# Optimization experiments

Measured on AMD Instinct MI355X. Metric: run time of the kernel, lower is better.

Reference implementation:

```python
import jax, jax.numpy as jnp
import numpy as np

B, T, D, H = 4, 2048, 1024, 16
DH = D // H  # 64
EPS = 1e-5


def _layernorm(x, g, b):
    mu = jnp.mean(x, axis=-1, keepdims=True)
    var = jnp.var(x, axis=-1, keepdims=True)
    return (x - mu) * jax.lax.rsqrt(var + EPS) * g + b


def setup_inputs() -> dict:
    key = jax.random.key(0)
    ks = jax.random.split(key, 12)
    s = 0.02
    x = jax.random.normal(ks[0], (B, T, D), dtype=jnp.float32)
    # causal mask (the repo registers tril as the eos_mask buffer)
    eos_mask = jnp.broadcast_to(jnp.tril(jnp.ones((T, T), dtype=jnp.int32)), (B, T, T))
    Wq = jax.random.normal(ks[1], (H, D, DH), dtype=jnp.float32) * s
    Wk = jax.random.normal(ks[2], (H, D, DH), dtype=jnp.float32) * s
    Wv = jax.random.normal(ks[3], (H, D, DH), dtype=jnp.float32) * s
    Wp = jax.random.normal(ks[4], (D, D), dtype=jnp.float32) * s
    bp = jnp.zeros((D,), dtype=jnp.float32)
    W1 = jax.random.normal(ks[5], (D, 4 * D), dtype=jnp.float32) * s
    b1 = jnp.zeros((4 * D,), dtype=jnp.float32)
    W2 = jax.random.normal(ks[6], (4 * D, D), dtype=jnp.float32) * s
    b2 = jnp.zeros((D,), dtype=jnp.float32)
    g1 = jnp.ones((D,), dtype=jnp.float32)
    beta1 = jnp.zeros((D,), dtype=jnp.float32)
    g2 = jnp.ones((D,), dtype=jnp.float32)
    beta2 = jnp.zeros((D,), dtype=jnp.float32)
    return dict(x=x, eos_mask=eos_mask, Wq=Wq, Wk=Wk, Wv=Wv, Wp=Wp, bp=bp,
                W1=W1, b1=b1, W2=W2, b2=b2, g1=g1, beta1=beta1, g2=g2, beta2=beta2)


def reference(x, eos_mask, Wq, Wk, Wv, Wp, bp, W1, b1, W2, b2, g1, beta1, g2, beta2):
    # x: [B,T,D]; eos_mask: [B,T,T]
    x1 = _layernorm(x, g1, beta1)
    q = jnp.einsum('btd,hdk->bhtk', x1, Wq)
    k = jnp.einsum('btd,hdk->bhtk', x1, Wk)
    v = jnp.einsum('btd,hdk->bhtk', x1, Wv)
    # NOTE: original scales by 1/sqrt(C) where C = d_model (not d_head)
    scores = jnp.einsum('bhtk,bhsk->bhts', q, k) / np.sqrt(x.shape[-1]).astype(np.float32)
    scores = jnp.where(eos_mask[:, None, :, :] == 0, jnp.float32(-jnp.inf), scores)
    wei = jax.nn.softmax(scores, axis=-1)
    attn = jnp.einsum('bhts,bhsk->bhtk', wei, v)          # [B,H,T,DH]
    attn = attn.transpose(0, 2, 1, 3).reshape(x.shape)    # concat heads -> [B,T,D]
    attn = attn @ Wp + bp
    x2 = x1 + attn
    x3 = _layernorm(x2, g2, beta2)
    mlp = jax.nn.relu(x3 @ W1 + b1) @ W2 + b2
    out = x3 + mlp
    return out
```

## Files before the change

kernel.cpp:

```cpp
#include <hip/hip_runtime.h>


#define B_ 4
#define T_ 2048
#define D_ 1024
#define H_ 16
#define DH_ 64

using u16 = unsigned short;
typedef short bf16x8 __attribute__((ext_vector_type(8)));
typedef float f32x4 __attribute__((ext_vector_type(4)));

#define GLOAD_LDS16(g, l)                                                          \
  __builtin_amdgcn_global_load_lds((const __attribute__((address_space(1))) void*)(g), \
                                   (__attribute__((address_space(3))) void*)(l), 16, 0, 0)

#define CVTPK(d, lo, hi) asm("v_cvt_pk_bf16_f32 %0, %1, %2" : "=v"(d) : "v"(lo), "v"(hi))
#define BARSB() do { __builtin_amdgcn_s_barrier(); __builtin_amdgcn_sched_barrier(0); } while (0)

__device__ __forceinline__ f32x4 mfma16(bf16x8 a, bf16x8 b, f32x4 c) {
  return __builtin_amdgcn_mfma_f32_16x16x32_bf16(a, b, c, 0, 0, 0);
}

__device__ __forceinline__ u16 f2bf(float f) {
  union { float f; unsigned u; } v; v.f = f;
  unsigned r = v.u + 0x7fffu + ((v.u >> 16) & 1u);
  return (u16)(r >> 16);
}
__device__ __forceinline__ float bf2f(u16 h) {
  union { unsigned u; float f; } v; v.u = ((unsigned)h) << 16; return v.f;
}

template<typename TI>
__global__ __launch_bounds__(256)
void ln_kernel(const TI* __restrict__ x, const float* __restrict__ g,
               const float* __restrict__ be, u16* __restrict__ yb)
{
  const int row = blockIdx.x;
  const int tid = threadIdx.x;
  float v0, v1, v2, v3;
  if constexpr (sizeof(TI) == 4) {
    const float4 vx = ((const float4*)(x + (size_t)row * D_))[tid];
    v0 = vx.x; v1 = vx.y; v2 = vx.z; v3 = vx.w;
  } else {
    const ushort4 vx = ((const ushort4*)((const u16*)x + (size_t)row * D_))[tid];
    v0 = bf2f(vx.x); v1 = bf2f(vx.y); v2 = bf2f(vx.z); v3 = bf2f(vx.w);
  }
  float s  = v0 + v1 + v2 + v3;
  float s2 = v0*v0 + v1*v1 + v2*v2 + v3*v3;
#pragma unroll
  for (int m = 1; m < 64; m <<= 1) { s += __shfl_xor(s, m); s2 += __shfl_xor(s2, m); }
  __shared__ float red[8];
  const int w = tid >> 6;
  if ((tid & 63) == 0) { red[w] = s; red[4 + w] = s2; }
  __syncthreads();
  s  = red[0] + red[1] + red[2] + red[3];
  s2 = red[4] + red[5] + red[6] + red[7];
  const float mu   = s * (1.0f / D_);
  const float rstd = rsqrtf(s2 * (1.0f / D_) - mu * mu + 1e-5f);
  const float4 gg = ((const float4*)g)[tid];
  const float4 bb = ((const float4*)be)[tid];
  ushort4 pk;
  pk.x = f2bf((v0 - mu) * rstd * gg.x + bb.x);
  pk.y = f2bf((v1 - mu) * rstd * gg.y + bb.y);
  pk.z = f2bf((v2 - mu) * rstd * gg.z + bb.z);
  pk.w = f2bf((v3 - mu) * rstd * gg.w + bb.w);
  ((ushort4*)(yb + (size_t)row * D_))[tid] = pk;
}

__global__ __launch_bounds__(256)
void transpose_cvt(const float* __restrict__ in, u16* __restrict__ out, int R, int C)
{
  __shared__ float tile[32][33];
  const int c0 = blockIdx.x * 32, r0 = blockIdx.y * 32;
  const float* ip = in + (size_t)blockIdx.z * R * C;
  u16* op = out + (size_t)blockIdx.z * R * C;
  const int tx = threadIdx.x, ty = threadIdx.y;
#pragma unroll
  for (int j = 0; j < 4; ++j)
    tile[ty + j * 8][tx] = ip[(size_t)(r0 + ty + j * 8) * C + (c0 + tx)];
  __syncthreads();
#pragma unroll
  for (int j = 0; j < 4; ++j)
    op[(size_t)(c0 + ty + j * 8) * R + (r0 + tx)] = f2bf(tile[tx][ty + j * 8]);
}

#define MODE_QKV 0
#define MODE_WP 1
#define MODE_MLP1 2
#define MODE_MLP2 3

template<int MODE>
__global__ __launch_bounds__(512, 2)
void gemm256v2(const u16* __restrict__ A, const u16* __restrict__ Bt,
               int M, int N, int K,
               const float* __restrict__ bias, const u16* __restrict__ resid,
               float* __restrict__ outf, u16* __restrict__ outb,
               u16* __restrict__ qo, u16* __restrict__ ko, u16* __restrict__ vo)
{
  __shared__ __align__(16) u16 Ash[2][256 * 64];
  __shared__ __align__(16) u16 Bsh[2][256 * 64];
  const int t = threadIdx.x, w = t >> 6, l = t & 63, lg = l >> 4, lr = l & 15;
  const int wr = w >> 2, wc = w & 3;

  const int gx = gridDim.x;
  const int nwg = gx * gridDim.y;
  const int bid = blockIdx.y * gx + blockIdx.x;
  const int cpx = nwg >> 3;
  const int virt = (bid & 7) * cpx + (bid >> 3);
  const int bn0 = (virt % gx) * 256, bm0 = (virt / gx) * 256;

  f32x4 acc[8][4] = {};

  const int srow = t >> 3;
  const int sc16 = (t & 7) ^ (srow & 7);
  const u16* gAs = A  + (size_t)(bm0 + srow) * K + sc16 * 8;
  const u16* gBs = Bt + (size_t)(bn0 + srow) * K + sc16 * 8;

#define ISS2_A(R, BUF, ko) GLOAD_LDS16(gAs + (size_t)(R) * 64 * K + (ko), &Ash[BUF][(R) * 4096 + w * 512])
#define ISS2_B(R, BUF, ko) GLOAD_LDS16(gBs + (size_t)(R) * 64 * K + (ko), &Bsh[BUF][(R) * 4096 + w * 512])

  const int nkt = K >> 6;
  ISS2_A(0, 0, 0); ISS2_A(1, 0, 0); ISS2_A(2, 0, 0); ISS2_A(3, 0, 0);
  ISS2_B(0, 0, 0); ISS2_B(1, 0, 0); ISS2_B(2, 0, 0); ISS2_B(3, 0, 0);
  if (nkt > 1) {
    ISS2_A(0, 1, 64); ISS2_A(1, 1, 64);
    asm volatile("s_waitcnt vmcnt(2)" ::: "memory");
  } else {
    asm volatile("s_waitcnt vmcnt(0)" ::: "memory");
  }
  BARSB();

  auto rdA = [&](int buf, int m) -> bf16x8 {
    const int r = wr * 128 + m * 16 + lr;
    return *(const bf16x8*)((const char*)&Ash[buf][0] + r * 128 + (((0 + lg) ^ (r & 7)) << 4));
  };
  auto rdA1 = [&](int buf, int m) -> bf16x8 {
    const int r = wr * 128 + m * 16 + lr;
    return *(const bf16x8*)((const char*)&Ash[buf][0] + r * 128 + (((4 + lg) ^ (r & 7)) << 4));
  };
  auto rdB0 = [&](int buf, int n) -> bf16x8 {
    const int r = wc * 64 + n * 16 + lr;
    return *(const bf16x8*)((const char*)&Bsh[buf][0] + r * 128 + (((0 + lg) ^ (r & 7)) << 4));
  };
  auto rdB1 = [&](int buf, int n) -> bf16x8 {
    const int r = wc * 64 + n * 16 + lr;
    return *(const bf16x8*)((const char*)&Bsh[buf][0] + r * 128 + (((4 + lg) ^ (r & 7)) << 4));
  };

  bf16x8 afr[4][2], bfr[4][2];

  for (int i = 0; i < nkt; ++i) {
    const int buf = i & 1, nb = buf ^ 1;
    const size_t k1 = (size_t)(i + 1) << 6, k2 = (size_t)(i + 2) << 6;
    const bool n1 = (i + 1 < nkt), n2 = (i + 2 < nkt);

#pragma unroll
    for (int m = 0; m < 4; ++m) { afr[m][0] = rdA(buf, m); afr[m][1] = rdA1(buf, m); }
#pragma unroll
    for (int n = 0; n < 2; ++n) { bfr[n][0] = rdB0(buf, n); bfr[n][1] = rdB1(buf, n); }
    if (n1) { ISS2_A(2, nb, k1); ISS2_A(3, nb, k1); }
    BARSB();
    __builtin_amdgcn_s_setprio(1);
#pragma unroll
    for (int m = 0; m < 4; ++m)
#pragma unroll
      for (int n = 0; n < 2; ++n) {
        acc[m][n] = mfma16(afr[m][0], bfr[n][0], acc[m][n]);
        acc[m][n] = mfma16(afr[m][1], bfr[n][1], acc[m][n]);
      }
    __builtin_amdgcn_s_setprio(0);
    BARSB();

#pragma unroll
    for (int n = 2; n < 4; ++n) { bfr[n][0] = rdB0(buf, n); bfr[n][1] = rdB1(buf, n); }
    if (n1) { ISS2_B(0, nb, k1); ISS2_B(1, nb, k1); }
    BARSB();
    __builtin_amdgcn_s_setprio(1);
#pragma unroll
    for (int m = 0; m < 4; ++m)
#pragma unroll
      for (int n = 2; n < 4; ++n) {
        acc[m][n] = mfma16(afr[m][0], bfr[n][0], acc[m][n]);
        acc[m][n] = mfma16(afr[m][1], bfr[n][1], acc[m][n]);
      }
    __builtin_amdgcn_s_setprio(0);
    BARSB();

#pragma unroll
    for (int m = 0; m < 4; ++m) { afr[m][0] = rdA(buf, 4 + m); afr[m][1] = rdA1(buf, 4 + m); }
    if (n1) { ISS2_B(2, nb, k1); ISS2_B(3, nb, k1); }
    BARSB();
    __builtin_amdgcn_s_setprio(1);
#pragma unroll
    for (int m = 0; m < 4; ++m)
#pragma unroll
      for (int n = 0; n < 2; ++n) {
        acc[4 + m][n] = mfma16(afr[m][0], bfr[n][0], acc[4 + m][n]);
        acc[4 + m][n] = mfma16(afr[m][1], bfr[n][1], acc[4 + m][n]);
      }
    __builtin_amdgcn_s_setprio(0);
    BARSB();

    if (n2) { ISS2_A(0, buf, k2); ISS2_A(1, buf, k2); }
    BARSB();
    __builtin_amdgcn_s_setprio(1);
#pragma unroll
    for (int m = 0; m < 4; ++m)
#pragma unroll
      for (int n = 2; n < 4; ++n) {
        acc[4 + m][n] = mfma16(afr[m][0], bfr[n][0], acc[4 + m][n]);
        acc[4 + m][n] = mfma16(afr[m][1], bfr[n][1], acc[4 + m][n]);
      }
    __builtin_amdgcn_s_setprio(0);
    if (n2) asm volatile("s_waitcnt vmcnt(2)" ::: "memory");
    else    asm volatile("s_waitcnt vmcnt(0)" ::: "memory");
    BARSB();
  }
#undef ISS2_A
#undef ISS2_B

#pragma unroll
  for (int m = 0; m < 8; ++m) {
#pragma unroll
    for (int n = 0; n < 4; ++n) {
#pragma unroll
      for (int r = 0; r < 4; ++r) {
        const int row = bm0 + wr * 128 + m * 16 + lg * 4 + r;
        const int col = bn0 + wc * 64 + n * 16 + lr;
        float v = acc[m][n][r];
        if constexpr (MODE == MODE_QKV) {
          const int sel = col >> 10, hh = (col >> 6) & 15, dh = col & 63;
          const int bi = row >> 11, tt = row & 2047;
          u16* dst = (sel == 0) ? qo : (sel == 1) ? ko : vo;
          dst[(((size_t)bi * H_ + hh) * T_ + tt) * DH_ + dh] = f2bf(v);
        } else if constexpr (MODE == MODE_MLP1) {
          v += bias[col];
          outb[(size_t)row * N + col] = f2bf(v > 0.f ? v : 0.f);
        }
      }
    }
  }
}

template<int MODE>
__global__ __launch_bounds__(512, 4)
void gemm128(const u16* __restrict__ A, const u16* __restrict__ Bt,
             int M, int N, int K,
             const float* __restrict__ bias, const u16* __restrict__ resid,
             float* __restrict__ outf, u16* __restrict__ outb,
             u16* __restrict__ qo, u16* __restrict__ ko, u16* __restrict__ vo)
{
  __shared__ __align__(16) u16 Ash[2][128 * 64];
  __shared__ __align__(16) u16 Bsh[2][128 * 64];
  const int t = threadIdx.x, w = t >> 6, l = t & 63, lg = l >> 4, lr = l & 15;
  const int wr = w >> 2, wc = w & 3;

  const int gx = gridDim.x;
  const int nwg = gx * gridDim.y;
  const int bid = blockIdx.y * gx + blockIdx.x;
  const int cpx = nwg >> 3;
  const int virt = (bid & 7) * cpx + (bid >> 3);
  const int bn0 = (virt % gx) * 128, bm0 = (virt / gx) * 128;

  f32x4 acc[4][2] = {};

  const int srow = t >> 3;
  const int sc16 = (t & 7) ^ (srow & 7);
  const u16* gAs = A  + (size_t)(bm0 + srow) * K + sc16 * 8;
  const u16* gBs = Bt + (size_t)(bn0 + srow) * K + sc16 * 8;

#define ISS_A(R, BUF, ko) GLOAD_LDS16(gAs + (size_t)(R) * 64 * K + (ko), &Ash[BUF][(R) * 4096 + w * 512])
#define ISS_B(R, BUF, ko) GLOAD_LDS16(gBs + (size_t)(R) * 64 * K + (ko), &Bsh[BUF][(R) * 4096 + w * 512])

  ISS_A(0, 0, 0); ISS_A(1, 0, 0); ISS_B(0, 0, 0); ISS_B(1, 0, 0);
  ISS_A(0, 1, 64); ISS_A(1, 1, 64); ISS_B(0, 1, 64); ISS_B(1, 1, 64);

  auto rdA = [&](int buf, int m, int kk) -> bf16x8 {
    const int r = wr * 64 + m * 16 + lr;
    return *(const bf16x8*)((const char*)&Ash[buf][0] + r * 128 + (((kk * 4 + lg) ^ (r & 7)) << 4));
  };
  auto rdB = [&](int buf, int n, int kk) -> bf16x8 {
    const int r = wc * 32 + n * 16 + lr;
    return *(const bf16x8*)((const char*)&Bsh[buf][0] + r * 128 + (((kk * 4 + lg) ^ (r & 7)) << 4));
  };

  const int nkt = K >> 6;
  for (int i = 0; i < nkt; ++i) {
    const int buf = i & 1;
    if (i + 1 < nkt) asm volatile("s_waitcnt vmcnt(4)" ::: "memory");
    else             asm volatile("s_waitcnt vmcnt(0)" ::: "memory");
    BARSB();

    bf16x8 afr[4][2], bfr[2][2];
#pragma unroll
    for (int m = 0; m < 4; ++m) { afr[m][0] = rdA(buf, m, 0); afr[m][1] = rdA(buf, m, 1); }
#pragma unroll
    for (int n = 0; n < 2; ++n) { bfr[n][0] = rdB(buf, n, 0); bfr[n][1] = rdB(buf, n, 1); }

    __builtin_amdgcn_s_setprio(1);
#pragma unroll
    for (int m = 0; m < 4; ++m)
#pragma unroll
      for (int n = 0; n < 2; ++n) {
        acc[m][n] = mfma16(afr[m][0], bfr[n][0], acc[m][n]);
        acc[m][n] = mfma16(afr[m][1], bfr[n][1], acc[m][n]);
      }
    __builtin_amdgcn_s_setprio(0);
    BARSB();

    if (i + 2 < nkt) {
      const size_t ko = (size_t)(i + 2) << 6;
      ISS_A(0, buf, ko); ISS_A(1, buf, ko); ISS_B(0, buf, ko); ISS_B(1, buf, ko);
    }
  }
#undef ISS_A
#undef ISS_B

#pragma unroll
  for (int m = 0; m < 4; ++m) {
#pragma unroll
    for (int n = 0; n < 2; ++n) {
#pragma unroll
      for (int r = 0; r < 4; ++r) {
        const int row = bm0 + wr * 64 + m * 16 + lg * 4 + r;
        const int col = bn0 + wc * 32 + n * 16 + lr;
        float v = acc[m][n][r];
        if constexpr (MODE == MODE_WP) {
          v += bias[col] + bf2f(resid[(size_t)row * N + col]);
          outb[(size_t)row * N + col] = f2bf(v);
        } else if constexpr (MODE == MODE_MLP2) {
          outf[(size_t)row * N + col] = v + bias[col] + bf2f(resid[(size_t)row * N + col]);
        }
      }
    }
  }
}

__global__ __launch_bounds__(256, 2)
void attn_kernel(const u16* __restrict__ q, const u16* __restrict__ k,
                 const u16* __restrict__ v, u16* __restrict__ out)
{
  __shared__ __align__(16) u16 Ks[2][4096];
  __shared__ __align__(16) u16 Vt[2][4096];
  const int t = threadIdx.x, w = t >> 6, l = t & 63, lg = l >> 4, lr = l & 15;

  const int bid = blockIdx.x;
  const int virt = (bid & 7) * 256 + (bid >> 3);
  const int bh = (virt >> 8) * 8 + (virt & 7);
  const int qt = 31 - ((virt >> 3) & 31);

  const int b = bh >> 4, h = bh & 15;
  const u16* Qp = q + (size_t)bh * T_ * DH_;
  const u16* Kp = k + (size_t)bh * T_ * DH_;
  const u16* Vp = v + (size_t)bh * T_ * DH_;

  const int qrow = qt * 64 + w * 16 + lr;
  const bf16x8 qf0 = *(const bf16x8*)&Qp[(size_t)qrow * DH_ + lg * 8];
  const bf16x8 qf1 = *(const bf16x8*)&Qp[(size_t)qrow * DH_ + 32 + lg * 8];

  const int srow = t >> 3;
  const int kcol = (((t & 7) ^ (srow & 7)) << 3);
  const int vdh0 = (t & 7) << 3;
  const u16* Kg = Kp + (size_t)srow * DH_ + kcol;
  const u16* Vg = Vp + (size_t)srow * DH_ + vdh0;

  float m_run = -1e30f, l_run = 0.f;
  f32x4 o[4] = {};
  const float SC2 = 0.03125f * 1.44269504f;
  const float THR2 = 11.5416f;

  auto writeV = [&](int buf, uint4 va, uint4 vb) {
    const u16* pa = (const u16*)&va;
    const u16* pb = (const u16*)&vb;
    char* base = (char*)&Vt[buf][0];
#pragma unroll
    for (int j = 0; j < 8; ++j) {
      const int dh = vdh0 + j;
      const int swz = (((dh & 7) ^ ((dh >> 3) & 7)) << 4);
      *(u16*)(base + (((dh << 7) + (srow << 1)) ^ swz)) = pa[j];
      *(u16*)(base + (((dh << 7) + ((32 + srow) << 1)) ^ swz)) = pb[j];
    }
  };

  GLOAD_LDS16(Kg,            &Ks[0][w * 512]);
  GLOAD_LDS16(Kg + 32 * DH_, &Ks[0][2048 + w * 512]);
  {
    uint4 v0 = *(const uint4*)Vg;
    uint4 v1 = *(const uint4*)(Vg + 32 * DH_);
    writeV(0, v0, v1);
  }
  __syncthreads();

  const int nst = qt + 1;
  for (int st = 0; st < nst; ++st) {
    const int cur = st & 1, nxt = cur ^ 1;
    uint4 vA, vB;
    const bool pf = (st + 1 < nst);
    if (pf) {
      const u16* kg = Kg + (size_t)(st + 1) * 64 * DH_;
      GLOAD_LDS16(kg,            &Ks[nxt][w * 512]);
      GLOAD_LDS16(kg + 32 * DH_, &Ks[nxt][2048 + w * 512]);
      vA = *(const uint4*)(Vg + (size_t)(st + 1) * 64 * DH_);
      vB = *(const uint4*)(Vg + (size_t)(st + 1) * 64 * DH_ + 32 * DH_);
    }

    f32x4 sa[4] = {};
    const char* kb = (const char*)&Ks[cur][0];
    __builtin_amdgcn_s_setprio(1);
#pragma unroll
    for (int n = 0; n < 4; ++n) {
      const int sr = n * 16 + lr;
      const int base = (sr << 7) + (lg << 4);
      const int swz = (sr & 7) << 4;
      const bf16x8 b0 = *(const bf16x8*)(kb + (base ^ swz));
      const bf16x8 b1 = *(const bf16x8*)(kb + ((base + 64) ^ swz));
      sa[n] = mfma16(b0, qf0, sa[n]);
      sa[n] = mfma16(b1, qf1, sa[n]);
    }
    __builtin_amdgcn_s_setprio(0);

    float sc[4][4];
    float rm = -1e30f;
#pragma unroll
    for (int n = 0; n < 4; ++n)
#pragma unroll
      for (int r = 0; r < 4; ++r) {
        float x = sa[n][r] * SC2;
        if (st == qt && (st * 64 + n * 16 + lg * 4 + r) > qrow) x = -1e30f;
        sc[n][r] = x;
        rm = fmaxf(rm, x);
      }
    rm = fmaxf(rm, __shfl_xor(rm, 16));
    rm = fmaxf(rm, __shfl_xor(rm, 32));
    const bool noresc = __all(rm <= m_run + THR2);
    if (!noresc) {
      const float mnew = fmaxf(m_run, rm);
      const float al = exp2f(m_run - mnew);
      m_run = mnew;
      l_run *= al;
      const float alr0 = __shfl(al, lg * 4 + 0);
      const float alr1 = __shfl(al, lg * 4 + 1);
      const float alr2 = __shfl(al, lg * 4 + 2);
      const float alr3 = __shfl(al, lg * 4 + 3);
#pragma unroll
      for (int n = 0; n < 4; ++n) {
        o[n][0] *= alr0; o[n][1] *= alr1; o[n][2] *= alr2; o[n][3] *= alr3;
      }
    }
    float p[4][4];
    float rs = 0.f;
#pragma unroll
    for (int n = 0; n < 4; ++n)
#pragma unroll
      for (int r = 0; r < 4; ++r) {
        p[n][r] = exp2f(sc[n][r] - m_run);
        rs += p[n][r];
      }
    rs += __shfl_xor(rs, 16);
    rs += __shfl_xor(rs, 32);
    l_run += rs;

    unsigned pk0a, pk0b, pk1a, pk1b, pk2a, pk2b, pk3a, pk3b;
    CVTPK(pk0a, p[0][0], p[0][1]); CVTPK(pk0b, p[0][2], p[0][3]);
    CVTPK(pk1a, p[1][0], p[1][1]); CVTPK(pk1b, p[1][2], p[1][3]);
    CVTPK(pk2a, p[2][0], p[2][1]); CVTPK(pk2b, p[2][2], p[2][3]);
    CVTPK(pk3a, p[3][0], p[3][1]); CVTPK(pk3b, p[3][2], p[3][3]);

    const int srcA = lr + ((l >> 4) & 1) * 32;
    const int srcB = srcA + 16;
    const bool hi = (l >> 5) & 1;
    union { uint4 u; bf16x8 v8; } f0, f1;
    {
      const unsigned xA0 = __shfl(pk0a, srcA), xA1 = __shfl(pk0b, srcA);
      const unsigned yA0 = __shfl(pk1a, srcA), yA1 = __shfl(pk1b, srcA);
      const unsigned xB0 = __shfl(pk0a, srcB), xB1 = __shfl(pk0b, srcB);
      const unsigned yB0 = __shfl(pk1a, srcB), yB1 = __shfl(pk1b, srcB);
      f0.u.x = hi ? yA0 : xA0; f0.u.y = hi ? yA1 : xA1;
      f0.u.z = hi ? yB0 : xB0; f0.u.w = hi ? yB1 : xB1;
    }
    {
      const unsigned xA0 = __shfl(pk2a, srcA), xA1 = __shfl(pk2b, srcA);
      const unsigned yA0 = __shfl(pk3a, srcA), yA1 = __shfl(pk3b, srcA);
      const unsigned xB0 = __shfl(pk2a, srcB), xB1 = __shfl(pk2b, srcB);
      const unsigned yB0 = __shfl(pk3a, srcB), yB1 = __shfl(pk3b, srcB);
      f1.u.x = hi ? yA0 : xA0; f1.u.y = hi ? yA1 : xA1;
      f1.u.z = hi ? yB0 : xB0; f1.u.w = hi ? yB1 : xB1;
    }

    const char* vbase = (const char*)&Vt[cur][0];
    __builtin_amdgcn_s_setprio(1);
#pragma unroll
    for (int ks = 0; ks < 2; ++ks) {
      const bf16x8 pa = ks ? f1.v8 : f0.v8;
#pragma unroll
      for (int n = 0; n < 4; ++n) {
        const int dh = n * 16 + lr;
        int vbyte = (dh << 7) + (ks << 6) + (lg << 4);
        vbyte ^= (((dh & 7) ^ ((dh >> 3) & 7)) << 4);
        const bf16x8 vbf = *(const bf16x8*)(vbase + vbyte);
        o[n] = mfma16(pa, vbf, o[n]);
      }
    }
    __builtin_amdgcn_s_setprio(0);

    if (pf) writeV(nxt, vA, vB);
    __syncthreads();
  }

  const size_t obase = ((size_t)b * T_) * D_ + (size_t)h * DH_;
  float li[4];
  li[0] = 1.0f / __shfl(l_run, lg * 4 + 0);
  li[1] = 1.0f / __shfl(l_run, lg * 4 + 1);
  li[2] = 1.0f / __shfl(l_run, lg * 4 + 2);
  li[3] = 1.0f / __shfl(l_run, lg * 4 + 3);
#pragma unroll
  for (int n = 0; n < 4; ++n) {
#pragma unroll
    for (int r = 0; r < 4; ++r) {
      const int qg = qt * 64 + w * 16 + lg * 4 + r;
      out[obase + (size_t)qg * D_ + n * 16 + lr] = f2bf(o[n][r] * li[r]);
    }
  }
}

extern "C" void kernel_launch(void* const* d_in, const int* in_sizes, int n_in,
                              void* d_out, int out_size, void* d_ws, size_t ws_size,
                              hipStream_t stream) {
  (void)in_sizes; (void)n_in; (void)out_size; (void)ws_size;
  const float* x   = (const float*)d_in[0];
  const float* Wq  = (const float*)d_in[2];
  const float* Wk  = (const float*)d_in[3];
  const float* Wv  = (const float*)d_in[4];
  const float* Wp  = (const float*)d_in[5];
  const float* bp  = (const float*)d_in[6];
  const float* W1  = (const float*)d_in[7];
  const float* b1  = (const float*)d_in[8];
  const float* W2  = (const float*)d_in[9];
  const float* b2  = (const float*)d_in[10];
  const float* g1  = (const float*)d_in[11];
  const float* be1 = (const float*)d_in[12];
  const float* g2  = (const float*)d_in[13];
  const float* be2 = (const float*)d_in[14];

  char* ws = (char*)d_ws;
  const size_t MB16 = 16777216;
  u16* x1b   = (u16*)(ws);
  u16* qb    = (u16*)(ws + 1 * MB16);
  u16* kb    = (u16*)(ws + 2 * MB16);
  u16* vb    = (u16*)(ws + 3 * MB16);
  u16* attnb = (u16*)(ws + 4 * MB16);
  u16* x2b   = (u16*)(ws + 5 * MB16);
  u16* hb    = (u16*)(ws + 6 * MB16);
  u16* wqkvb = (u16*)(ws + 10 * MB16);
  u16* wpb   = (u16*)(ws + 10 * MB16 + 6291456);
  u16* w1b   = (u16*)(ws + 10 * MB16 + 8388608);
  u16* w2b   = (u16*)(ws + 11 * MB16);
  u16* x3b   = qb;

  dim3 tb(32, 8, 1);
  transpose_cvt<<<dim3(2, 32, 16),  tb, 0, stream>>>(Wq, wqkvb,                    1024, 64);
  transpose_cvt<<<dim3(2, 32, 16),  tb, 0, stream>>>(Wk, wqkvb + (size_t)1048576,  1024, 64);
  transpose_cvt<<<dim3(2, 32, 16),  tb, 0, stream>>>(Wv, wqkvb + (size_t)2097152,  1024, 64);
  transpose_cvt<<<dim3(32, 32, 1),  tb, 0, stream>>>(Wp, wpb, 1024, 1024);
  transpose_cvt<<<dim3(128, 32, 1), tb, 0, stream>>>(W1, w1b, 1024, 4096);
  transpose_cvt<<<dim3(32, 128, 1), tb, 0, stream>>>(W2, w2b, 4096, 1024);

  ln_kernel<float><<<8192, 256, 0, stream>>>(x, g1, be1, x1b);

  gemm256v2<MODE_QKV><<<dim3(12, 32), 512, 0, stream>>>(
      x1b, wqkvb, 8192, 3072, 1024, nullptr, nullptr, nullptr, nullptr, qb, kb, vb);

  attn_kernel<<<dim3(2048), 256, 0, stream>>>(qb, kb, vb, attnb);

  gemm128<MODE_WP><<<dim3(8, 64), 512, 0, stream>>>(
      attnb, wpb, 8192, 1024, 1024, bp, x1b, nullptr, x2b, nullptr, nullptr, nullptr);

  ln_kernel<u16><<<8192, 256, 0, stream>>>(x2b, g2, be2, x3b);

  gemm256v2<MODE_MLP1><<<dim3(16, 32), 512, 0, stream>>>(
      x3b, w1b, 8192, 4096, 1024, b1, nullptr, nullptr, hb, nullptr, nullptr, nullptr);

  gemm128<MODE_MLP2><<<dim3(8, 64), 512, 0, stream>>>(
      hb, w2b, 8192, 1024, 4096, b2, x3b, (float*)d_out, nullptr, nullptr, nullptr, nullptr);
}
```

Measured before the change: 370.7 us.

## Pre-transpose V in a separate kernel and load it into LDS asynchronously

Adds a bf16 transpose kernel that writes V as [bh, DH, T] into a reused workspace buffer. The attention kernel can then fetch V tiles with direct global-to-LDS loads, the same way it fetches K, replacing register loads followed by scattered 2-byte LDS stores. This is meant to remove the per-tile transpose cost and the register pressure inside the attention loop. In exchange it adds an extra kernel launch and a full read and write of V in global memory.

```diff
diff --git a/kernel.cpp b/kernel.cpp
--- a/kernel.cpp
+++ b/kernel.cpp
@@ -85,6 +85,23 @@
     op[(size_t)(c0 + ty + j * 8) * R + (r0 + tx)] = f2bf(tile[tx][ty + j * 8]);
 }
 
+__global__ __launch_bounds__(256)
+void transpose_bf(const u16* __restrict__ in, u16* __restrict__ out, int R, int C)
+{
+  __shared__ u16 tile[32][34];
+  const int c0 = blockIdx.x * 32, r0 = blockIdx.y * 32;
+  const u16* ip = in + (size_t)blockIdx.z * R * C;
+  u16* op = out + (size_t)blockIdx.z * R * C;
+  const int tx = threadIdx.x, ty = threadIdx.y;
+#pragma unroll
+  for (int j = 0; j < 4; ++j)
+    tile[ty + j * 8][tx] = ip[(size_t)(r0 + ty + j * 8) * C + (c0 + tx)];
+  __syncthreads();
+#pragma unroll
+  for (int j = 0; j < 4; ++j)
+    op[(size_t)(c0 + ty + j * 8) * R + (r0 + tx)] = tile[tx][ty + j * 8];
+}
+
 #define MODE_QKV 0
 #define MODE_WP 1
 #define MODE_MLP1 2
@@ -339,10 +356,10 @@
 
 __global__ __launch_bounds__(256, 2)
 void attn_kernel(const u16* __restrict__ q, const u16* __restrict__ k,
-                 const u16* __restrict__ v, u16* __restrict__ out)
+                 const u16* __restrict__ vt, u16* __restrict__ out)
 {
   __shared__ __align__(16) u16 Ks[2][4096];
-  __shared__ __align__(16) u16 Vt[2][4096];
+  __shared__ __align__(16) u16 Vs[2][4096];
   const int t = threadIdx.x, w = t >> 6, l = t & 63, lg = l >> 4, lr = l & 15;
 
   const int bid = blockIdx.x;
@@ -351,58 +368,41 @@
   const int qt = 31 - ((virt >> 3) & 31);
 
   const int b = bh >> 4, h = bh & 15;
-  const u16* Qp = q + (size_t)bh * T_ * DH_;
-  const u16* Kp = k + (size_t)bh * T_ * DH_;
-  const u16* Vp = v + (size_t)bh * T_ * DH_;
+  const u16* Qp  = q  + (size_t)bh * T_ * DH_;
+  const u16* Kp  = k  + (size_t)bh * T_ * DH_;
+  const u16* Vtp = vt + (size_t)bh * T_ * DH_;
 
   const int qrow = qt * 64 + w * 16 + lr;
   const bf16x8 qf0 = *(const bf16x8*)&Qp[(size_t)qrow * DH_ + lg * 8];
   const bf16x8 qf1 = *(const bf16x8*)&Qp[(size_t)qrow * DH_ + 32 + lg * 8];
 
   const int srow = t >> 3;
-  const int kcol = (((t & 7) ^ (srow & 7)) << 3);
-  const int vdh0 = (t & 7) << 3;
-  const u16* Kg = Kp + (size_t)srow * DH_ + kcol;
-  const u16* Vg = Vp + (size_t)srow * DH_ + vdh0;
+  const int schunk = ((t & 7) ^ (srow & 7)) << 3;
+  const u16* Kg = Kp  + (size_t)srow * DH_ + schunk;
+  const u16* Vg = Vtp + (size_t)srow * T_  + schunk;
 
   float m_run = -1e30f, l_run = 0.f;
   f32x4 o[4] = {};
   const float SC2 = 0.03125f * 1.44269504f;
   const float THR2 = 11.5416f;
 
-  auto writeV = [&](int buf, uint4 va, uint4 vb) {
-    const u16* pa = (const u16*)&va;
-    const u16* pb = (const u16*)&vb;
-    char* base = (char*)&Vt[buf][0];
-#pragma unroll
-    for (int j = 0; j < 8; ++j) {
-      const int dh = vdh0 + j;
-      const int swz = (((dh & 7) ^ ((dh >> 3) & 7)) << 4);
-      *(u16*)(base + (((dh << 7) + (srow << 1)) ^ swz)) = pa[j];
-      *(u16*)(base + (((dh << 7) + ((32 + srow) << 1)) ^ swz)) = pb[j];
-    }
-  };
-
   GLOAD_LDS16(Kg,            &Ks[0][w * 512]);
   GLOAD_LDS16(Kg + 32 * DH_, &Ks[0][2048 + w * 512]);
-  {
-    uint4 v0 = *(const uint4*)Vg;
-    uint4 v1 = *(const uint4*)(Vg + 32 * DH_);
-    writeV(0, v0, v1);
-  }
+  GLOAD_LDS16(Vg,            &Vs[0][w * 512]);
+  GLOAD_LDS16(Vg + 32 * T_,  &Vs[0][2048 + w * 512]);
   __syncthreads();
 
   const int nst = qt + 1;
   for (int st = 0; st < nst; ++st) {
     const int cur = st & 1, nxt = cur ^ 1;
-    uint4 vA, vB;
     const bool pf = (st + 1 < nst);
     if (pf) {
       const u16* kg = Kg + (size_t)(st + 1) * 64 * DH_;
+      const u16* vg = Vg + (size_t)(st + 1) * 64;
       GLOAD_LDS16(kg,            &Ks[nxt][w * 512]);
       GLOAD_LDS16(kg + 32 * DH_, &Ks[nxt][2048 + w * 512]);
-      vA = *(const uint4*)(Vg + (size_t)(st + 1) * 64 * DH_);
-      vB = *(const uint4*)(Vg + (size_t)(st + 1) * 64 * DH_ + 32 * DH_);
+      GLOAD_LDS16(vg,            &Vs[nxt][w * 512]);
+      GLOAD_LDS16(vg + 32 * T_,  &Vs[nxt][2048 + w * 512]);
     }
 
     f32x4 sa[4] = {};
@@ -488,7 +488,7 @@
       f1.u.z = hi ? yB0 : xB0; f1.u.w = hi ? yB1 : xB1;
     }
 
-    const char* vbase = (const char*)&Vt[cur][0];
+    const char* vbase = (const char*)&Vs[cur][0];
     __builtin_amdgcn_s_setprio(1);
 #pragma unroll
     for (int ks = 0; ks < 2; ++ks) {
@@ -496,15 +496,14 @@
 #pragma unroll
       for (int n = 0; n < 4; ++n) {
         const int dh = n * 16 + lr;
-        int vbyte = (dh << 7) + (ks << 6) + (lg << 4);
-        vbyte ^= (((dh & 7) ^ ((dh >> 3) & 7)) << 4);
-        const bf16x8 vbf = *(const bf16x8*)(vbase + vbyte);
+        const int base = (dh << 7) + (ks << 6) + (lg << 4);
+        const int swz = (dh & 7) << 4;
+        const bf16x8 vbf = *(const bf16x8*)(vbase + (base ^ swz));
         o[n] = mfma16(pa, vbf, o[n]);
       }
     }
     __builtin_amdgcn_s_setprio(0);
 
-    if (pf) writeV(nxt, vA, vB);
     __syncthreads();
   }
 
@@ -552,6 +551,7 @@
   u16* attnb = (u16*)(ws + 4 * MB16);
   u16* x2b   = (u16*)(ws + 5 * MB16);
   u16* hb    = (u16*)(ws + 6 * MB16);
+  u16* vtb   = hb;
   u16* wqkvb = (u16*)(ws + 10 * MB16);
   u16* wpb   = (u16*)(ws + 10 * MB16 + 6291456);
   u16* w1b   = (u16*)(ws + 10 * MB16 + 8388608);
@@ -571,7 +571,9 @@
   gemm256v2<MODE_QKV><<<dim3(12, 32), 512, 0, stream>>>(
       x1b, wqkvb, 8192, 3072, 1024, nullptr, nullptr, nullptr, nullptr, qb, kb, vb);
 
-  attn_kernel<<<dim3(2048), 256, 0, stream>>>(qb, kb, vb, attnb);
+  transpose_bf<<<dim3(2, 64, 64), tb, 0, stream>>>(vb, vtb, 2048, 64);
+
+  attn_kernel<<<dim3(2048), 256, 0, stream>>>(qb, kb, vtb, attnb);
 
   gemm128<MODE_WP><<<dim3(8, 64), 512, 0, stream>>>(
       attnb, wpb, 8192, 1024, 1024, bp, x1b, nullptr, x2b, nullptr, nullptr, nullptr);
```

Result: no change. 375.0 us (+1.2%).
